# Optimization experiments

Measured on AMD Instinct MI355X. Metric: run time of the kernel, lower is better.

Reference implementation:

```python
import jax, jax.numpy as jnp
import numpy as np

B, L_TXT, L_IMG = 1, 256, 2048
D_MODEL, HEADS, DIM_HEAD = 2048, 16, 128
S = L_TXT + L_IMG
QMAX = 127.0  # int8 symmetric
SM_SCALE = 1.0 / float(np.sqrt(DIM_HEAD))


def quant_act(x):
    # dynamic per-tensor symmetric int8 fake-quant with straight-through estimator
    scale = jnp.maximum(jnp.max(jnp.abs(x)) / QMAX, 1e-8)
    q = jnp.clip(jnp.round(x / scale), -QMAX, QMAX) * scale
    return x + jax.lax.stop_gradient(q - x)


def quant_weight(w):
    # per-output-channel symmetric int8 fake-quant (STE)
    scale = jnp.maximum(jnp.max(jnp.abs(w), axis=1, keepdims=True) / QMAX, 1e-8)
    q = jnp.clip(jnp.round(w / scale), -QMAX, QMAX) * scale
    return w + jax.lax.stop_gradient(q - w)


def qlinear(x, w, b):
    return x @ quant_weight(w).T + b


def rmsnorm(x, w, eps=1e-6):
    var = jnp.mean(jnp.square(x), axis=-1, keepdims=True)
    return x * jax.lax.rsqrt(var + eps) * w


def apply_rope(x, cos, sin):
    # diffusers apply_rotary_emb, use_real with interleaved (real, imag) pairs
    xr = x.reshape(*x.shape[:-1], -1, 2)
    rot = jnp.stack([-xr[..., 1], xr[..., 0]], axis=-1).reshape(x.shape)
    return x * cos + rot * sin


def heads_split(x):
    # [B, L, H*D] -> [B, H, L, D]
    return x.reshape(B, -1, HEADS, DIM_HEAD).transpose(0, 2, 1, 3)


def setup_inputs() -> dict:
    key = jax.random.key(0)
    ks = jax.random.split(key, 12)
    inp = {
        'hidden_states': jax.random.normal(ks[0], (B, L_IMG, D_MODEL), jnp.float32),
        'encoder_hidden_states': jax.random.normal(ks[1], (B, L_TXT, D_MODEL), jnp.float32),
    }
    freqs = 1.0 / (10000.0 ** (jnp.arange(0, DIM_HEAD, 2, dtype=jnp.float32) / DIM_HEAD))
    ang = jnp.arange(S, dtype=jnp.float32)[:, None] * freqs[None, :]  # [S, D/2]
    inp['rope_cos'] = jnp.repeat(jnp.cos(ang), 2, axis=-1)  # [S, D]
    inp['rope_sin'] = jnp.repeat(jnp.sin(ang), 2, axis=-1)
    wn = ['wq', 'wk', 'wv', 'w_add_q', 'w_add_k', 'w_add_v', 'w_out', 'w_add_out']
    bn = ['bq', 'bk', 'bv', 'b_add_q', 'b_add_k', 'b_add_v', 'b_out', 'b_add_out']
    for i, (w, b) in enumerate(zip(wn, bn)):
        inp[w] = jax.random.normal(ks[2 + i], (D_MODEL, D_MODEL), jnp.float32) * 0.02
        inp[b] = jnp.zeros((D_MODEL,), jnp.float32)
    for n in ['norm_q_w', 'norm_k_w', 'norm_added_q_w', 'norm_added_k_w']:
        inp[n] = jnp.ones((DIM_HEAD,), jnp.float32)
    return inp


def reference(hidden_states, encoder_hidden_states, rope_cos, rope_sin,
              wq, bq, wk, bk, wv, bv,
              w_add_q, b_add_q, w_add_k, b_add_k, w_add_v, b_add_v,
              w_out, b_out, w_add_out, b_add_out,
              norm_q_w, norm_k_w, norm_added_q_w, norm_added_k_w):
    # image-token branch
    h = quant_act(hidden_states)
    q = heads_split(qlinear(h, wq, bq))
    k = heads_split(qlinear(h, wk, bk))
    v = heads_split(qlinear(h, wv, bv))
    q = quant_act(rmsnorm(q, norm_q_w))
    k = quant_act(rmsnorm(k, norm_k_w))
    v = quant_act(v)
    # text-token (encoder) branch
    e = quant_act(encoder_hidden_states)
    eq = heads_split(qlinear(e, w_add_q, b_add_q))
    ek = heads_split(qlinear(e, w_add_k, b_add_k))
    ev = heads_split(qlinear(e, w_add_v, b_add_v))
    eq = quant_act(rmsnorm(eq, norm_added_q_w))
    ek = quant_act(rmsnorm(ek, norm_added_k_w))
    ev = quant_act(ev)
    # joint sequence: [text; image]
    q = jnp.concatenate([eq, q], axis=2)
    k = jnp.concatenate([ek, k], axis=2)
    v = jnp.concatenate([ev, v], axis=2)
    cos = rope_cos[None, None]
    sin = rope_sin[None, None]
    q = apply_rope(q, cos, sin)
    k = apply_rope(k, cos, sin)
    scores = jnp.einsum('bhqd,bhkd->bhqk', q, k) * SM_SCALE
    probs = jax.nn.softmax(scores, axis=-1)
    out = jnp.einsum('bhqk,bhkd->bhqd', probs, v)
    out = out.transpose(0, 2, 1, 3).reshape(B, S, HEADS * DIM_HEAD)
    out = quant_act(out)
    enc, img = out[:, :L_TXT], out[:, L_TXT:]
    img = qlinear(img, w_out, b_out)
    enc = qlinear(enc, w_add_out, b_add_out)
    return (img, enc)
```

## Files before the change

kernel.cpp:

```cpp
#include <hip/hip_runtime.h>

constexpr int L_TXT = 256, L_IMG = 2048, SEQ = 2304;
constexpr int DM = 2048, NH = 16, DH = 128;
constexpr int NSPLIT = 4;
constexpr int SSTR = 32;

typedef __attribute__((ext_vector_type(8))) __bf16 bf16x8;
typedef __attribute__((ext_vector_type(4))) float f32x4;

__device__ __forceinline__ float ldin(const void* p, size_t i, int bf) {
  return bf ? (float)((const __bf16*)p)[i] : ((const float*)p)[i];
}
__device__ __forceinline__ float slot_scale(const unsigned* s) {
  return fmaxf(__uint_as_float(*s) / 127.0f, 1e-8f);
}
__device__ __forceinline__ float qclamp(float x, float sc) {
  float q = rintf(x / sc);
  return fminf(fmaxf(q, -127.0f), 127.0f);
}
__device__ __forceinline__ float block_allmax_n(float v) {
  #pragma unroll
  for (int off = 32; off; off >>= 1) v = fmaxf(v, __shfl_xor(v, off));
  __shared__ float sm[16];
  int nw = blockDim.x >> 6;
  __syncthreads();
  if ((threadIdx.x & 63) == 0) sm[threadIdx.x >> 6] = v;
  __syncthreads();
  float m = sm[0];
  for (int i = 1; i < nw; i++) m = fmaxf(m, sm[i]);
  return m;
}

__global__ void detect_k(const void* cosp, int* flag) {
  if (threadIdx.x == 0) *flag = (((const unsigned short*)cosp)[0] != 0) ? 1 : 0;
}

struct Ptrs8 { const void* p[8]; };

__global__ void quant_weights_k(Ptrs8 win, __bf16* __restrict__ wq, float* __restrict__ scales,
                                const int* __restrict__ flagp) {
  const int bf = *flagp;
  int row = blockIdx.x, mat = blockIdx.y, t = threadIdx.x;
  float v[8];
  if (bf) {
    union { int4 q; __bf16 h[8]; } u;
    u.q = ((const int4*)((const __bf16*)win.p[mat] + (size_t)row * DM))[t];
    #pragma unroll
    for (int j = 0; j < 8; j++) v[j] = (float)u.h[j];
  } else {
    const float4* p = (const float4*)((const float*)win.p[mat] + (size_t)row * DM);
    float4 a = p[t * 2], b = p[t * 2 + 1];
    v[0]=a.x; v[1]=a.y; v[2]=a.z; v[3]=a.w; v[4]=b.x; v[5]=b.y; v[6]=b.z; v[7]=b.w;
  }
  float m = 0.f;
  #pragma unroll
  for (int j = 0; j < 8; j++) m = fmaxf(m, fabsf(v[j]));
  m = block_allmax_n(m);
  float sc = fmaxf(m / 127.0f, 1e-8f);
  if (t == 0) scales[mat * DM + row] = sc;
  union { int4 q; __bf16 h[8]; } o;
  #pragma unroll
  for (int j = 0; j < 8; j++) o.h[j] = (__bf16)qclamp(v[j], sc);
  ((int4*)(wq + (size_t)mat * DM * DM + (size_t)row * DM))[t] = o.q;
}
__global__ void weight_scales_k(Ptrs8 win, float* __restrict__ scales, const int* __restrict__ flagp) {
  const int bf = *flagp;
  int row = blockIdx.x, mat = blockIdx.y, t = threadIdx.x;
  float m = 0.f;
  for (int c = t; c < DM; c += 256) m = fmaxf(m, fabsf(ldin(win.p[mat], (size_t)row * DM + c, bf)));
  m = block_allmax_n(m);
  if (t == 0) scales[mat * DM + row] = fmaxf(m / 127.0f, 1e-8f);
}

__global__ void absmax_he_k(const void* __restrict__ hs, const void* __restrict__ es,
                            unsigned* s0, unsigned* s1, const int* __restrict__ flagp) {
  const int bf = *flagp;
  const int n18 = L_IMG * DM / 8, n28 = L_TXT * DM / 8;
  float m1 = 0.f, m2 = 0.f;
  for (int i = blockIdx.x * 256 + threadIdx.x; i < n18 + n28; i += gridDim.x * 256) {
    bool h = i < n18;
    const void* src = h ? hs : es;
    int j = h ? i : i - n18;
    float lm = 0.f;
    if (bf) {
      union { int4 q; __bf16 x[8]; } u; u.q = ((const int4*)src)[j];
      #pragma unroll
      for (int k = 0; k < 8; k++) lm = fmaxf(lm, fabsf((float)u.x[k]));
    } else {
      const float4* p = (const float4*)src;
      float4 a = p[j * 2], b = p[j * 2 + 1];
      lm = fmaxf(fmaxf(fmaxf(fabsf(a.x), fabsf(a.y)), fmaxf(fabsf(a.z), fabsf(a.w))),
                 fmaxf(fmaxf(fabsf(b.x), fabsf(b.y)), fmaxf(fabsf(b.z), fabsf(b.w))));
    }
    if (h) m1 = fmaxf(m1, lm); else m2 = fmaxf(m2, lm);
  }
  m1 = block_allmax_n(m1);
  __syncthreads();
  m2 = block_allmax_n(m2);
  if (threadIdx.x == 0) { atomicMax(s0, __float_as_uint(m1)); atomicMax(s1, __float_as_uint(m2)); }
}

__global__ void quant_he_k(const void* __restrict__ hs, const void* __restrict__ es,
                           const unsigned* __restrict__ slots, __bf16* __restrict__ hqo,
                           __bf16* __restrict__ eqo, const int* __restrict__ flagp) {
  const int bf = *flagp;
  const int n18 = L_IMG * DM / 8, n28 = L_TXT * DM / 8;
  float sc0 = slot_scale(slots), sc1 = slot_scale(slots + SSTR);
  for (int i = blockIdx.x * 256 + threadIdx.x; i < n18 + n28; i += gridDim.x * 256) {
    bool h = i < n18;
    const void* src = h ? hs : es;
    int j = h ? i : i - n18;
    float sc = h ? sc0 : sc1;
    float v[8];
    if (bf) {
      union { int4 q; __bf16 x[8]; } u; u.q = ((const int4*)src)[j];
      #pragma unroll
      for (int k = 0; k < 8; k++) v[k] = (float)u.x[k];
    } else {
      const float4* p = (const float4*)src;
      float4 a = p[j * 2], b = p[j * 2 + 1];
      v[0]=a.x; v[1]=a.y; v[2]=a.z; v[3]=a.w; v[4]=b.x; v[5]=b.y; v[6]=b.z; v[7]=b.w;
    }
    union { int4 q; __bf16 x[8]; } o;
    #pragma unroll
    for (int k = 0; k < 8; k++) o.x[k] = (__bf16)qclamp(v[k], sc);
    ((int4*)(h ? hqo : eqo))[j] = o.q;
  }
}

__global__ void quant_f32x8_k(const float* __restrict__ x, int n8,
                              const unsigned* __restrict__ slot, __bf16* __restrict__ out) {
  float sc = slot_scale(slot);
  for (int i = blockIdx.x * 256 + threadIdx.x; i < n8; i += gridDim.x * 256) {
    float4 a = ((const float4*)x)[i * 2], b = ((const float4*)x)[i * 2 + 1];
    union { int4 q; __bf16 h[8]; } o;
    o.h[0]=(__bf16)qclamp(a.x,sc); o.h[1]=(__bf16)qclamp(a.y,sc);
    o.h[2]=(__bf16)qclamp(a.z,sc); o.h[3]=(__bf16)qclamp(a.w,sc);
    o.h[4]=(__bf16)qclamp(b.x,sc); o.h[5]=(__bf16)qclamp(b.y,sc);
    o.h[6]=(__bf16)qclamp(b.z,sc); o.h[7]=(__bf16)qclamp(b.w,sc);
    ((int4*)out)[i] = o.q;
  }
}
__global__ void absmax_f32_k(const float* __restrict__ x, int n, unsigned* slot) {
  float m = 0.f;
  for (int i = blockIdx.x * 256 + threadIdx.x; i < n; i += gridDim.x * 256)
    m = fmaxf(m, fabsf(x[i]));
  m = block_allmax_n(m);
  if (threadIdx.x == 0) atomicMax(slot, __float_as_uint(m));
}

__global__ void rms_absmax_v_k(float* __restrict__ qf, float* __restrict__ kf, float* __restrict__ vf,
                               const void* nq, const void* naq, const void* nk, const void* nak,
                               unsigned* __restrict__ slots, const int* __restrict__ flagp) {
  const int bf = *flagp;
  const int t = threadIdx.x, lane = t & 63, wave = t >> 6;
  float wqt0 = ldin(naq, lane, bf), wqt1 = ldin(naq, lane + 64, bf);
  float wqi0 = ldin(nq,  lane, bf), wqi1 = ldin(nq,  lane + 64, bf);
  float wkt0 = ldin(nak, lane, bf), wkt1 = ldin(nak, lane + 64, bf);
  float wki0 = ldin(nk,  lane, bf), wki1 = ldin(nk,  lane + 64, bf);
  const int NR = NH * SEQ;
  float mx[6] = {0.f, 0.f, 0.f, 0.f, 0.f, 0.f};
  for (int row = blockIdx.x * 16 + wave; row < 3 * NR; row += gridDim.x * 16) {
    int tns = row / NR, r2 = row - tns * NR;
    int s = r2 % SEQ; bool txt = s < L_TXT;
    float* p = (tns == 0 ? qf : tns == 1 ? kf : vf) + (size_t)r2 * DH;
    float v0 = p[lane], v1 = p[lane + 64];
    if (tns < 2) {
      float ss = v0 * v0 + v1 * v1;
      #pragma unroll
      for (int off = 32; off; off >>= 1) ss += __shfl_xor(ss, off);
      float r = rsqrtf(ss * (1.0f / 128.0f) + 1e-6f);
      float w0, w1;
      if (tns == 0) { w0 = txt ? wqt0 : wqi0; w1 = txt ? wqt1 : wqi1; }
      else          { w0 = txt ? wkt0 : wki0; w1 = txt ? wkt1 : wki1; }
      v0 *= r * w0; v1 *= r * w1;
      p[lane] = v0; p[lane + 64] = v1;
    }
    int idx = tns * 2 + (txt ? 0 : 1);
    mx[idx] = fmaxf(mx[idx], fmaxf(fabsf(v0), fabsf(v1)));
  }
  #pragma unroll
  for (int off = 32; off; off >>= 1)
    #pragma unroll
    for (int j = 0; j < 6; j++) mx[j] = fmaxf(mx[j], __shfl_xor(mx[j], off));
  __shared__ float smx[16][6];
  if (lane == 0)
    #pragma unroll
    for (int j = 0; j < 6; j++) smx[wave][j] = mx[j];
  __syncthreads();
  if (t == 0) {
    #pragma unroll
    for (int j = 0; j < 6; j++) {
      float m = smx[0][j];
      for (int i = 1; i < 16; i++) m = fmaxf(m, smx[i][j]);
      atomicMax(slots + (2 + j) * SSTR, __float_as_uint(m));
    }
  }
}

__global__ void rope2_k(const float* __restrict__ qf, const float* __restrict__ kf,
                        const void* cosb, const void* sinb, const unsigned* __restrict__ slots,
                        __bf16* __restrict__ qb, __bf16* __restrict__ kb, const int* __restrict__ flagp) {
  const int bf = *flagp;
  const int NP = NH * SEQ * 64;
  for (int i = blockIdx.x * 256 + threadIdx.x; i < 2 * NP; i += gridDim.x * 256) {
    int tns = i >= NP;
    int j = i - tns * NP;
    int pr = j & 63, rowg = j >> 6;
    int s = rowg % SEQ;
    const float* src = tns ? kf : qf;
    __bf16* dst = tns ? kb : qb;
    float sc = slot_scale(slots + (tns ? 4 : 2) * SSTR + (s < L_TXT ? 0 : SSTR));
    size_t base = (size_t)rowg * DH + pr * 2;
    float2 x2 = *(const float2*)(src + base);
    float q0 = qclamp(x2.x, sc) * sc, q1 = qclamp(x2.y, sc) * sc;
    float c0 = ldin(cosb, s * DH + 2 * pr, bf), c1 = ldin(cosb, s * DH + 2 * pr + 1, bf);
    float s0 = ldin(sinb, s * DH + 2 * pr, bf), s1 = ldin(sinb, s * DH + 2 * pr + 1, bf);
    dst[base]     = (__bf16)(q0 * c0 - q1 * s0);
    dst[base + 1] = (__bf16)(q1 * c1 + q0 * s1);
  }
}

__global__ void quant_transpose_v_k(const float* __restrict__ v, const unsigned* __restrict__ slots,
                                    __bf16* __restrict__ vt) {
  __shared__ float tile[64][65];
  int t = threadIdx.x;
  int s0 = blockIdx.x * 64, d0 = blockIdx.y * 64, h = blockIdx.z;
  #pragma unroll
  for (int i = 0; i < 16; i++) {
    int r = i * 4 + (t >> 6), c = t & 63;
    tile[r][c] = v[((size_t)(h * SEQ) + s0 + r) * DH + d0 + c];
  }
  __syncthreads();
  float sc = slot_scale(slots + (s0 < L_TXT ? 6 : 7) * SSTR);
  #pragma unroll
  for (int i = 0; i < 16; i++) {
    int d = i * 4 + (t >> 6), s = t & 63;
    float q = qclamp(tile[s][d], sc) * sc;
    vt[((size_t)(h * DH) + d0 + d) * SEQ + s0 + s] = (__bf16)q;
  }
}

struct GemmArgs {
  const __bf16 *hq, *eq, *attnq;
  const __bf16* wqp;
  const void* Wraw[8];
  const float* wsc;
  const void* bias[8];
  float* outs[3];
  void* dout;
  const unsigned* slots;
  const int* flagp;
};
template<int MODE, int QW>
__global__ __launch_bounds__(256, 2)
void gemm_f(GemmArgs a) {
  const int bf = *a.flagp;
  constexpr int K = DM;
  __shared__ __bf16 As[128][72];
  __shared__ __bf16 Ws[128][72];
  const int t = threadIdx.x, lane = t & 63, wave = t >> 6;
  const int l15 = lane & 15, quad = lane >> 4;
  const int n0 = blockIdx.x * 128, y = blockIdx.y;
  int mat, outrow; const __bf16* A; const unsigned* aslot;
  if (MODE == 0) {
    bool txt = y < 2;
    mat = blockIdx.z + (txt ? 3 : 0);
    A = (txt ? a.eq : a.hq) + (size_t)(txt ? y * 128 : (y - 2) * 128) * K;
    outrow = y * 128;
    aslot = a.slots + (txt ? SSTR : 0);
  } else {
    bool img = y < 16;
    mat = img ? 6 : 7;
    A = a.attnq + (size_t)(img ? L_TXT + y * 128 : (y - 16) * 128) * K;
    outrow = img ? y * 128 : L_IMG + (y - 16) * 128;
    aslot = a.slots + 8 * SSTR;
  }
  const __bf16* Wq = QW ? a.wqp + (size_t)mat * DM * DM : nullptr;
  const void* Wr = a.Wraw[mat];
  const float* wrow = a.wsc + mat * DM;
  int wm = (wave & 1) * 64, wn = (wave >> 1) * 64;
  f32x4 acc[4][4] = {};
  int sr = t >> 3, sc = (t & 7) * 8;
  float wsc4[4];
  if (!QW) {
    #pragma unroll
    for (int p = 0; p < 4; p++) wsc4[p] = wrow[n0 + p * 32 + sr];
  }
  for (int k0 = 0; k0 < K; k0 += 64) {
    __syncthreads();
    #pragma unroll
    for (int p = 0; p < 4; p++) {
      int r = p * 32 + sr;
      *(int4*)&As[r][sc] = *(const int4*)&A[(size_t)r * K + k0 + sc];
      if (QW) {
        *(int4*)&Ws[r][sc] = *(const int4*)&Wq[(size_t)(n0 + r) * K + k0 + sc];
      } else {
        union { bf16x8 v; __bf16 h[8]; } q;
        if (bf) {
          union { int4 v; __bf16 h[8]; } u;
          u.v = *(const int4*)((const __bf16*)Wr + (size_t)(n0 + r) * K + k0 + sc);
          #pragma unroll
          for (int j = 0; j < 8; j++) q.h[j] = (__bf16)qclamp((float)u.h[j], wsc4[p]);
        } else {
          const float* wp = (const float*)Wr + (size_t)(n0 + r) * K + k0 + sc;
          float4 x = *(const float4*)wp, z = *(const float4*)(wp + 4);
          q.h[0]=(__bf16)qclamp(x.x,wsc4[p]); q.h[1]=(__bf16)qclamp(x.y,wsc4[p]);
          q.h[2]=(__bf16)qclamp(x.z,wsc4[p]); q.h[3]=(__bf16)qclamp(x.w,wsc4[p]);
          q.h[4]=(__bf16)qclamp(z.x,wsc4[p]); q.h[5]=(__bf16)qclamp(z.y,wsc4[p]);
          q.h[6]=(__bf16)qclamp(z.z,wsc4[p]); q.h[7]=(__bf16)qclamp(z.w,wsc4[p]);
        }
        *(bf16x8*)&Ws[r][sc] = q.v;
      }
    }
    __syncthreads();
    #pragma unroll
    for (int kk = 0; kk < 64; kk += 32) {
      bf16x8 af[4], bfr[4];
      #pragma unroll
      for (int i = 0; i < 4; i++) {
        af[i]  = *(const bf16x8*)&As[wm + i * 16 + l15][kk + quad * 8];
        bfr[i] = *(const bf16x8*)&Ws[wn + i * 16 + l15][kk + quad * 8];
      }
      #pragma unroll
      for (int i = 0; i < 4; i++)
        #pragma unroll
        for (int j = 0; j < 4; j++)
          acc[i][j] = __builtin_amdgcn_mfma_f32_16x16x32_bf16(af[i], bfr[j], acc[i][j], 0, 0, 0);
    }
  }
  float asc = slot_scale(aslot);
  #pragma unroll
  for (int j = 0; j < 4; j++) {
    int gn = n0 + wn + j * 16 + l15;
    float wsb = wrow[gn] * asc;
    float bv = ldin(a.bias[mat], gn, bf);
    #pragma unroll
    for (int i = 0; i < 4; i++)
      #pragma unroll
      for (int r = 0; r < 4; r++) {
        int gm = wm + i * 16 + quad * 4 + r;
        float val = acc[i][j][r] * wsb + bv;
        if (MODE == 0) {
          a.outs[blockIdx.z][(size_t)(gn >> 7) * (SEQ * DH) + (size_t)(outrow + gm) * DH + (gn & 127)] = val;
        } else {
          size_t idx = (size_t)(outrow + gm) * DM + gn;
          if (bf) ((__bf16*)a.dout)[idx] = (__bf16)val; else ((float*)a.dout)[idx] = val;
        }
      }
  }
}

template<int SPLIT>
__global__ __launch_bounds__(256)
void flash_attn_k(const __bf16* __restrict__ Qb, const __bf16* __restrict__ Kb,
                  const __bf16* __restrict__ Vt, float* __restrict__ O,
                  float* __restrict__ Op, float* __restrict__ Mp, float* __restrict__ Lp) {
  __shared__ __align__(16) char smem[9728 + 10240 + 5120];
  auto Ks = (__bf16(*)[152])smem;
  auto Vs = (__bf16(*)[40])(smem + 9728);
  auto Ps = (__bf16(*)[40])(smem + 9728 + 10240);
  const int t = threadIdx.x, lane = t & 63, wave = t >> 6;
  const int l15 = lane & 15, quad = lane >> 4;
  const int h = blockIdx.y, s0 = blockIdx.x * 64, qr = wave * 16;
  const float fscale = 0.08838834764831845f * 1.4426950408889634f;

  bf16x8 qf[4];
  #pragma unroll
  for (int kk = 0; kk < 4; kk++)
    qf[kk] = *(const bf16x8*)&Qb[(size_t)(h * SEQ + s0 + qr + l15) * DH + kk * 32 + quad * 8];

  f32x4 accO[8] = {};
  float m_st[4], l_st[4];
  #pragma unroll
  for (int r = 0; r < 4; r++) { m_st[r] = -1e30f; l_st[r] = 0.f; }

  const int NT = SEQ / 32;
  const int ktb = SPLIT ? blockIdx.z * (NT / NSPLIT) : 0;
  const int kte = SPLIT ? ktb + (NT / NSPLIT) : NT;

  const int krr = t >> 4, krc = (t & 15) * 8;
  const int vrr = t >> 2, vrc = (t & 3) * 8;
  int4 kreg[2], vreg[2];
  #pragma unroll
  for (int p = 0; p < 2; p++) {
    kreg[p] = *(const int4*)&Kb[(size_t)(h * SEQ + ktb * 32 + p * 16 + krr) * DH + krc];
    vreg[p] = *(const int4*)&Vt[(size_t)(h * DH + p * 64 + vrr) * SEQ + ktb * 32 + vrc];
  }

  for (int kt = ktb; kt < kte; kt++) {
    asm volatile("s_waitcnt lgkmcnt(0)" ::: "memory");
    __builtin_amdgcn_s_barrier();
    #pragma unroll
    for (int p = 0; p < 2; p++) {
      *(int4*)&Ks[p * 16 + krr][krc] = kreg[p];
      *(int4*)&Vs[p * 64 + vrr][vrc] = vreg[p];
    }
    if (kt + 1 < kte) {
      #pragma unroll
      for (int p = 0; p < 2; p++) {
        kreg[p] = *(const int4*)&Kb[(size_t)(h * SEQ + (kt + 1) * 32 + p * 16 + krr) * DH + krc];
        vreg[p] = *(const int4*)&Vt[(size_t)(h * DH + p * 64 + vrr) * SEQ + (kt + 1) * 32 + vrc];
      }
    }
    asm volatile("s_waitcnt lgkmcnt(0)" ::: "memory");
    __builtin_amdgcn_s_barrier();

    f32x4 accS[2] = {};
    __builtin_amdgcn_s_setprio(1);
    #pragma unroll
    for (int kk = 0; kk < 4; kk++)
      #pragma unroll
      for (int ni = 0; ni < 2; ni++) {
        bf16x8 bk = *(const bf16x8*)&Ks[ni * 16 + l15][kk * 32 + quad * 8];
        accS[ni] = __builtin_amdgcn_mfma_f32_16x16x32_bf16(qf[kk], bk, accS[ni], 0, 0, 0);
      }
    __builtin_amdgcn_s_setprio(0);

    #pragma unroll
    for (int r = 0; r < 4; r++) {
      float rm = fmaxf(accS[0][r], accS[1][r]);
      #pragma unroll
      for (int off = 8; off > 0; off >>= 1) rm = fmaxf(rm, __shfl_xor(rm, off));
      float mn = fmaxf(m_st[r], rm);
      float al = exp2f((m_st[r] - mn) * fscale);
      m_st[r] = mn;
      float rs = 0.f;
      #pragma unroll
      for (int ni = 0; ni < 2; ni++) {
        float pv = exp2f((accS[ni][r] - mn) * fscale);
        accS[ni][r] = pv;
        rs += pv;
      }
      #pragma unroll
      for (int off = 8; off > 0; off >>= 1) rs += __shfl_xor(rs, off);
      l_st[r] = l_st[r] * al + rs;
      #pragma unroll
      for (int di = 0; di < 8; di++)
        accO[di][r] *= al;
    }
    #pragma unroll
    for (int ni = 0; ni < 2; ni++)
      #pragma unroll
      for (int r = 0; r < 4; r++)
        Ps[qr + quad * 4 + r][ni * 16 + l15] = (__bf16)accS[ni][r];
    __builtin_amdgcn_s_setprio(1);
    {
      bf16x8 pa = *(const bf16x8*)&Ps[qr + l15][quad * 8];
      #pragma unroll
      for (int di = 0; di < 8; di++) {
        bf16x8 vb = *(const bf16x8*)&Vs[di * 16 + l15][quad * 8];
        accO[di] = __builtin_amdgcn_mfma_f32_16x16x32_bf16(pa, vb, accO[di], 0, 0, 0);
      }
    }
    __builtin_amdgcn_s_setprio(0);
  }
  if (SPLIT) {
    const size_t SP = (size_t)NH * SEQ * DH;
    const int sp = blockIdx.z;
    #pragma unroll
    for (int r = 0; r < 4; r++) {
      int gs = s0 + qr + quad * 4 + r;
      size_t ib = sp * SP + ((size_t)h * SEQ + gs) * DH;
      if (l15 == 0) {
        Mp[(size_t)sp * NH * SEQ + h * SEQ + gs] = m_st[r];
        Lp[(size_t)sp * NH * SEQ + h * SEQ + gs] = l_st[r];
      }
      #pragma unroll
      for (int di = 0; di < 8; di++)
        Op[ib + di * 16 + l15] = accO[di][r];
    }
  } else {
    #pragma unroll
    for (int r = 0; r < 4; r++) {
      float inv = 1.0f / l_st[r];
      int gs = s0 + qr + quad * 4 + r;
      #pragma unroll
      for (int di = 0; di < 8; di++)
        O[(size_t)gs * DM + h * DH + di * 16 + l15] = accO[di][r] * inv;
    }
  }
}

__global__ void flash_combine_k(const float* __restrict__ Op, const float* __restrict__ Mp,
                                const float* __restrict__ Lp, float* __restrict__ O,
                                unsigned* __restrict__ slot8) {
  const float fscale = 0.08838834764831845f * 1.4426950408889634f;
  const int t = threadIdx.x, lane = t & 63, w = t >> 6;
  const size_t SP = (size_t)NH * SEQ * DH, MR = (size_t)NH * SEQ;
  float lm = 0.f;
  for (int row = blockIdx.x * 16 + w; row < NH * SEQ; row += gridDim.x * 16) {
    float m0 = Mp[row], m1 = Mp[MR + row], m2 = Mp[2 * MR + row], m3 = Mp[3 * MR + row];
    float M = fmaxf(fmaxf(m0, m1), fmaxf(m2, m3));
    float w0 = exp2f((m0 - M) * fscale), w1 = exp2f((m1 - M) * fscale);
    float w2 = exp2f((m2 - M) * fscale), w3 = exp2f((m3 - M) * fscale);
    float inv = 1.0f / (Lp[row] * w0 + Lp[MR + row] * w1 + Lp[2 * MR + row] * w2 + Lp[3 * MR + row] * w3);
    int h = row / SEQ, s = row % SEQ;
    size_t ob = (size_t)s * DM + h * DH, ib = (size_t)row * DH;
    #pragma unroll
    for (int j = 0; j < 2; j++) {
      int d = lane + j * 64;
      float v = (Op[ib + d] * w0 + Op[SP + ib + d] * w1 +
                 Op[2 * SP + ib + d] * w2 + Op[3 * SP + ib + d] * w3) * inv;
      O[ob + d] = v;
      lm = fmaxf(lm, fabsf(v));
    }
  }
  lm = block_allmax_n(lm);
  if (t == 0) atomicMax(slot8, __float_as_uint(lm));
}

extern "C" void kernel_launch(void* const* d_in, const int* in_sizes, int n_in,
                              void* d_out, int out_size, void* d_ws, size_t ws_size,
                              hipStream_t stream) {
  (void)in_sizes; (void)n_in; (void)out_size;
  const void* hs   = d_in[0];
  const void* es   = d_in[1];
  const void* cosb = d_in[2];
  const void* sinb = d_in[3];
  const void* W[8]; const void* Bv[8];
  for (int i = 0; i < 8; i++) { W[i] = d_in[4 + 2 * i]; Bv[i] = d_in[5 + 2 * i]; }
  const void* nq  = d_in[20];
  const void* nk  = d_in[21];
  const void* naq = d_in[22];
  const void* nak = d_in[23];

  char* ws = (char*)d_ws;
  size_t off = 0;
  auto take = [&](size_t b) { char* p = ws + off; off += (b + 255) & ~(size_t)255; return p; };
  const size_t T = (size_t)NH * SEQ * DH * 4;

  unsigned* slots = (unsigned*)take(16 * SSTR * 4);
  int* flagp = (int*)(slots + 15 * SSTR);
  float* wsc = (float*)take(8ull * DM * 4);

  size_t here = off;
  size_t need_base  = 4 * T + T + 3 * (T / 2) + 2 * ((size_t)NSPLIT * NH * SEQ * 4 + 256) + 1024;
  bool do_split = here + need_base <= ws_size;
  size_t region_sz = do_split ? 4 * T : 3 * T;

  char* region = take(region_sz);
  float* qf = (float*)region;
  float* kf = (float*)(region + T);
  float* vf = (float*)(region + 2 * T);
  float* Opart = (float*)region;
  __bf16* attnq = (__bf16*)region;
  char* attnfR = take(T);
  __bf16* hq = (__bf16*)attnfR;
  __bf16* eq = (__bf16*)(attnfR + (size_t)L_IMG * DM * 2);
  float* attnf = (float*)attnfR;
  __bf16* qb  = (__bf16*)take(T / 2);
  __bf16* kb  = (__bf16*)take(T / 2);
  __bf16* vtb = (__bf16*)take(T / 2);
  float* Mpart = (float*)take((size_t)NSPLIT * NH * SEQ * 4);
  float* Lpart = (float*)take((size_t)NSPLIT * NH * SEQ * 4);
  bool do_prequant = (off + 8ull * DM * DM * 2 + 256 <= ws_size);
  __bf16* wq = do_prequant ? (__bf16*)take(8ull * DM * DM * 2) : nullptr;

  hipMemsetAsync(slots, 0, 16 * SSTR * 4, stream);
  detect_k<<<1, 64, 0, stream>>>(cosb, flagp);

  Ptrs8 win;
  for (int i = 0; i < 8; i++) win.p[i] = W[i];
  if (do_prequant)
    quant_weights_k<<<dim3(DM, 8), 256, 0, stream>>>(win, wq, wsc, flagp);
  else
    weight_scales_k<<<dim3(DM, 8), 256, 0, stream>>>(win, wsc, flagp);

  absmax_he_k<<<512, 256, 0, stream>>>(hs, es, slots, slots + SSTR, flagp);
  quant_he_k<<<1024, 256, 0, stream>>>(hs, es, slots, hq, eq, flagp);

  GemmArgs ga;
  ga.hq = hq; ga.eq = eq; ga.attnq = attnq; ga.wqp = wq;
  for (int i = 0; i < 8; i++) { ga.Wraw[i] = W[i]; ga.bias[i] = Bv[i]; }
  ga.wsc = wsc; ga.outs[0] = qf; ga.outs[1] = kf; ga.outs[2] = vf;
  ga.dout = d_out; ga.slots = slots; ga.flagp = flagp;

  if (do_prequant)
    gemm_f<0, 1><<<dim3(16, 18, 3), 256, 0, stream>>>(ga);
  else
    gemm_f<0, 0><<<dim3(16, 18, 3), 256, 0, stream>>>(ga);

  rms_absmax_v_k<<<256, 1024, 0, stream>>>(qf, kf, vf, nq, naq, nk, nak, slots, flagp);
  rope2_k<<<1024, 256, 0, stream>>>(qf, kf, cosb, sinb, slots, qb, kb, flagp);
  quant_transpose_v_k<<<dim3(SEQ / 64, DH / 64, NH), 256, 0, stream>>>(vf, slots, vtb);

  if (do_split) {
    flash_attn_k<1><<<dim3(SEQ / 64, NH, NSPLIT), 256, 0, stream>>>(qb, kb, vtb, nullptr,
                                                                    Opart, Mpart, Lpart);
    flash_combine_k<<<288, 1024, 0, stream>>>(Opart, Mpart, Lpart, attnf, slots + 8 * SSTR);
  } else {
    flash_attn_k<0><<<dim3(SEQ / 64, NH), 256, 0, stream>>>(qb, kb, vtb, attnf,
                                                            nullptr, nullptr, nullptr);
    absmax_f32_k<<<256, 256, 0, stream>>>(attnf, SEQ * DM, slots + 8 * SSTR);
  }
  quant_f32x8_k<<<1024, 256, 0, stream>>>(attnf, SEQ * DM / 8, slots + 8 * SSTR, attnq);

  if (do_prequant)
    gemm_f<1, 1><<<dim3(16, 18), 256, 0, stream>>>(ga);
  else
    gemm_f<1, 0><<<dim3(16, 18), 256, 0, stream>>>(ga);
}
```

Measured before the change: 718.5 us.

## Stage attention K/V tiles via direct global-to-LDS loads with double buffering

Replaces the register-staged K/V tile copy in the flash-attention kernel with `global_load_lds` DMA into two alternating LDS buffers. The bank-conflict padding is replaced by an XOR swizzle applied on the global-address side. This removes the VGPR round trip and one of the two barriers per tile, so the next tile's load can overlap the current tile's MFMA work. In exchange it doubles the K/V LDS footprint, which may reduce occupancy. Correctness also depends on the barrier waiting for outstanding LDS-DMA loads.

```diff
diff --git a/kernel.cpp b/kernel.cpp
--- a/kernel.cpp
+++ b/kernel.cpp
@@ -17,6 +17,11 @@
 __device__ __forceinline__ float qclamp(float x, float sc) {
   float q = rintf(x / sc);
   return fminf(fmaxf(q, -127.0f), 127.0f);
+}
+__device__ __forceinline__ void gload_lds16(const void* g, void* l) {
+  __builtin_amdgcn_global_load_lds(
+      (const __attribute__((address_space(1))) unsigned int*)g,
+      (__attribute__((address_space(3))) unsigned int*)l, 16, 0, 0);
 }
 __device__ __forceinline__ float block_allmax_n(float v) {
   #pragma unroll
@@ -356,10 +361,7 @@
 void flash_attn_k(const __bf16* __restrict__ Qb, const __bf16* __restrict__ Kb,
                   const __bf16* __restrict__ Vt, float* __restrict__ O,
                   float* __restrict__ Op, float* __restrict__ Mp, float* __restrict__ Lp) {
-  __shared__ __align__(16) char smem[9728 + 10240 + 5120];
-  auto Ks = (__bf16(*)[152])smem;
-  auto Vs = (__bf16(*)[40])(smem + 9728);
-  auto Ps = (__bf16(*)[40])(smem + 9728 + 10240);
+  __shared__ __align__(16) char smem[8192 * 4 + 5120];
   const int t = threadIdx.x, lane = t & 63, wave = t >> 6;
   const int l15 = lane & 15, quad = lane >> 4;
   const int h = blockIdx.y, s0 = blockIdx.x * 64, qr = wave * 16;
@@ -379,32 +381,43 @@
   const int ktb = SPLIT ? blockIdx.z * (NT / NSPLIT) : 0;
   const int kte = SPLIT ? ktb + (NT / NSPLIT) : NT;
 
-  const int krr = t >> 4, krc = (t & 15) * 8;
-  const int vrr = t >> 2, vrc = (t & 3) * 8;
-  int4 kreg[2], vreg[2];
-  #pragma unroll
-  for (int p = 0; p < 2; p++) {
-    kreg[p] = *(const int4*)&Kb[(size_t)(h * SEQ + ktb * 32 + p * 16 + krr) * DH + krc];
-    vreg[p] = *(const int4*)&Vt[(size_t)(h * DH + p * 64 + vrr) * SEQ + ktb * 32 + vrc];
-  }
-
+  int ldso[2], kgo[2], vgo[2];
+  #pragma unroll
+  for (int j = 0; j < 2; j++) {
+    int o = (wave * 2 + j) * 1024 + lane * 16;
+    ldso[j] = o;
+    int krow = o >> 8, kcp = o & 255;
+    kgo[j] = krow * 256 + (kcp ^ ((krow & 7) << 4));
+    int vrow = o >> 6, vcp = o & 63;
+    vgo[j] = vrow * (SEQ * 2) + (vcp ^ (((vrow >> 1) & 3) << 4));
+  }
+  const char* kgb = (const char*)Kb + (size_t)h * SEQ * (DH * 2);
+  const char* vgb = (const char*)Vt + (size_t)h * DH * (SEQ * 2);
+  const int kmask = (l15 & 7) << 4;
+  const int vmask = ((l15 >> 1) & 3) << 4;
+  __bf16* PsB = (__bf16*)(smem + 32768);
+
+  auto stage = [&](int buf, int kt) {
+    const char* ks = kgb + (size_t)kt * 8192;
+    char* kd = smem + buf * 8192;
+    #pragma unroll
+    for (int j = 0; j < 2; j++)
+      gload_lds16(ks + kgo[j], kd + ldso[j]);
+    const char* vs = vgb + (size_t)kt * 64;
+    char* vd = smem + 16384 + buf * 8192;
+    #pragma unroll
+    for (int j = 0; j < 2; j++)
+      gload_lds16(vs + vgo[j], vd + ldso[j]);
+  };
+
+  int cur = 0;
+  stage(0, ktb);
   for (int kt = ktb; kt < kte; kt++) {
-    asm volatile("s_waitcnt lgkmcnt(0)" ::: "memory");
-    __builtin_amdgcn_s_barrier();
-    #pragma unroll
-    for (int p = 0; p < 2; p++) {
-      *(int4*)&Ks[p * 16 + krr][krc] = kreg[p];
-      *(int4*)&Vs[p * 64 + vrr][vrc] = vreg[p];
-    }
-    if (kt + 1 < kte) {
-      #pragma unroll
-      for (int p = 0; p < 2; p++) {
-        kreg[p] = *(const int4*)&Kb[(size_t)(h * SEQ + (kt + 1) * 32 + p * 16 + krr) * DH + krc];
-        vreg[p] = *(const int4*)&Vt[(size_t)(h * DH + p * 64 + vrr) * SEQ + (kt + 1) * 32 + vrc];
-      }
-    }
-    asm volatile("s_waitcnt lgkmcnt(0)" ::: "memory");
-    __builtin_amdgcn_s_barrier();
+    __syncthreads();
+    if (kt + 1 < kte) stage(cur ^ 1, kt + 1);
+
+    const char* Kc = smem + cur * 8192;
+    const char* Vc = smem + 16384 + cur * 8192;
 
     f32x4 accS[2] = {};
     __builtin_amdgcn_s_setprio(1);
@@ -412,7 +425,7 @@
     for (int kk = 0; kk < 4; kk++)
       #pragma unroll
       for (int ni = 0; ni < 2; ni++) {
-        bf16x8 bk = *(const bf16x8*)&Ks[ni * 16 + l15][kk * 32 + quad * 8];
+        bf16x8 bk = *(const bf16x8*)(Kc + (ni * 16 + l15) * 256 + ((kk * 64 + quad * 16) ^ kmask));
         accS[ni] = __builtin_amdgcn_mfma_f32_16x16x32_bf16(qf[kk], bk, accS[ni], 0, 0, 0);
       }
     __builtin_amdgcn_s_setprio(0);
@@ -443,17 +456,18 @@
     for (int ni = 0; ni < 2; ni++)
       #pragma unroll
       for (int r = 0; r < 4; r++)
-        Ps[qr + quad * 4 + r][ni * 16 + l15] = (__bf16)accS[ni][r];
+        PsB[(qr + quad * 4 + r) * 40 + ni * 16 + l15] = (__bf16)accS[ni][r];
     __builtin_amdgcn_s_setprio(1);
     {
-      bf16x8 pa = *(const bf16x8*)&Ps[qr + l15][quad * 8];
+      bf16x8 pa = *(const bf16x8*)((const char*)PsB + (qr + l15) * 80 + quad * 16);
       #pragma unroll
       for (int di = 0; di < 8; di++) {
-        bf16x8 vb = *(const bf16x8*)&Vs[di * 16 + l15][quad * 8];
+        bf16x8 vb = *(const bf16x8*)(Vc + (di * 16 + l15) * 64 + ((quad * 16) ^ vmask));
         accO[di] = __builtin_amdgcn_mfma_f32_16x16x32_bf16(pa, vb, accO[di], 0, 0, 0);
       }
     }
     __builtin_amdgcn_s_setprio(0);
+    cur ^= 1;
   }
   if (SPLIT) {
     const size_t SP = (size_t)NH * SEQ * DH;
```

After: 653.0 us. 9.1% less time.
